# Kernel tuning notes

Hardware: AMD Instinct MI355X
Metric: run time of the kernel (lower is better)

## Reference

```python
import jax, jax.numpy as jnp
import numpy as np

D_MODEL = 1024
HEADS = 16
D_K = D_MODEL // HEADS


def setup_inputs() -> dict:
    key = jax.random.key(0)
    ks = jax.random.split(key, 12)
    B, S = 2, 2048
    scale = 1.0 / np.sqrt(D_MODEL)
    inp = {
        "q": jax.random.normal(ks[0], (B, S, D_MODEL), dtype=jnp.float32),
        "k": jax.random.normal(ks[1], (B, S, D_MODEL), dtype=jnp.float32),
        "v": jax.random.normal(ks[2], (B, S, D_MODEL), dtype=jnp.float32),
        "src_mask": jax.random.randint(ks[3], (B, 1, S), 0, 2, dtype=jnp.int32),
        # projection params (nn.Linear: y = x @ W.T + b); store W already transposed
        "Wq": jax.random.normal(ks[4], (D_MODEL, D_MODEL), dtype=jnp.float32) * scale,
        "bq": jnp.zeros((D_MODEL,), dtype=jnp.float32),
        "Wk": jax.random.normal(ks[5], (D_MODEL, D_MODEL), dtype=jnp.float32) * scale,
        "bk": jnp.zeros((D_MODEL,), dtype=jnp.float32),
        "Wv": jax.random.normal(ks[6], (D_MODEL, D_MODEL), dtype=jnp.float32) * scale,
        "bv": jnp.zeros((D_MODEL,), dtype=jnp.float32),
        "Wo": jax.random.normal(ks[7], (D_MODEL, D_MODEL), dtype=jnp.float32) * scale,
        "bo": jnp.zeros((D_MODEL,), dtype=jnp.float32),
    }
    return inp


def reference(q, k, v, src_mask, Wq, bq, Wk, bk, Wv, bv, Wo, bo):
    B, S, _ = q.shape
    # QKV projections, reshape to (b, heads, seq, d_k)
    def proj(x, W, b):
        y = x @ W + b  # (b, s, d_model)
        return y.reshape(B, S, HEADS, D_K).transpose(0, 2, 1, 3)

    qh = proj(q, Wq, bq)
    kh = proj(k, Wk, bk)
    vh = proj(v, Wv, bv)

    # scaled dot-product attention with padding mask
    scores = jnp.einsum("bhqd,bhkd->bhqk", qh, kh) / jnp.sqrt(jnp.float32(D_K))
    mask = src_mask[:, None, :, :]  # (b,1,1,s), broadcast over heads & query
    scores = jnp.where(mask == 0, jnp.float32(-1e9), scores)
    probs = jax.nn.softmax(scores, axis=-1)
    # dropout is identity in eval mode (reference baseline)
    ctx = jnp.einsum("bhqk,bhkd->bhqd", probs, vh)
    ctx = ctx.transpose(0, 2, 1, 3).reshape(B, S, D_MODEL)
    return ctx @ Wo + bo
```

## Files before the change

### kernel.cpp

```cpp
#include <hip/hip_runtime.h>
#include <hip/hip_bf16.h>

#define DM 1024
#define SL 2048
#define NH 16
#define DK 64

typedef __bf16 bf16;
typedef __bf16 bf16x8 __attribute__((ext_vector_type(8)));
typedef __bf16 bf16x4 __attribute__((ext_vector_type(4)));
typedef float f32x4 __attribute__((ext_vector_type(4)));
typedef float f32x16 __attribute__((ext_vector_type(16)));
typedef unsigned u32x4 __attribute__((ext_vector_type(4)));

__device__ __forceinline__ void gll16(const void* g, void* l) {
  __builtin_amdgcn_global_load_lds(
      (const __attribute__((address_space(1))) unsigned int*)g,
      (__attribute__((address_space(3))) unsigned int*)l, 16, 0, 0);
}

__device__ __forceinline__ unsigned pk2(float a, float b) {
  unsigned short lo = __builtin_bit_cast(unsigned short, (bf16)a);
  unsigned short hi = __builtin_bit_cast(unsigned short, (bf16)b);
  return (unsigned)lo | ((unsigned)hi << 16);
}

__global__ __launch_bounds__(256) void prep_kernel(
    const float* __restrict__ q, const float* __restrict__ k, const float* __restrict__ v,
    const float* __restrict__ Wq, const float* __restrict__ Wk,
    const float* __restrict__ Wv, const float* __restrict__ Wo,
    bf16* __restrict__ xq, bf16* __restrict__ xk, bf16* __restrict__ xv,
    bf16* __restrict__ TQ, bf16* __restrict__ TK, bf16* __restrict__ TV,
    bf16* __restrict__ TO) {
  __shared__ float t[64][65];
  const int bid = blockIdx.x, tid = threadIdx.x;
  if (bid < 6144) {
    const float* src; bf16* dst;
    if (bid < 2048)      { src = q; dst = xq; }
    else if (bid < 4096) { src = k; dst = xk; }
    else                 { src = v; dst = xv; }
    int i = (bid & 2047) * 2048 + tid * 8;
    f32x4 a = *(const f32x4*)(src + i);
    f32x4 b = *(const f32x4*)(src + i + 4);
    bf16x8 o;
    o[0]=(bf16)a[0]; o[1]=(bf16)a[1]; o[2]=(bf16)a[2]; o[3]=(bf16)a[3];
    o[4]=(bf16)b[0]; o[5]=(bf16)b[1]; o[6]=(bf16)b[2]; o[7]=(bf16)b[3];
    *(bf16x8*)(dst + i) = o;
  } else {
    const int wb = bid - 6144;
    const float* W; bf16* T;
    switch (wb >> 8) {
      case 0:  W = Wq; T = TQ; break;
      case 1:  W = Wk; T = TK; break;
      case 2:  W = Wv; T = TV; break;
      default: W = Wo; T = TO; break;
    }
    const int tile = wb & 255;
    const int tx = tile & 15, ty = tile >> 4;
    const int cr = tid >> 4, cc = tid & 15;
    #pragma unroll
    for (int rr = 0; rr < 4; ++rr) {
      int row = rr*16 + cr;
      f32x4 val = *(const f32x4*)(W + (ty*64 + row)*DM + tx*64 + cc*4);
      t[row][cc*4+0] = val[0]; t[row][cc*4+1] = val[1];
      t[row][cc*4+2] = val[2]; t[row][cc*4+3] = val[3];
    }
    __syncthreads();
    #pragma unroll
    for (int rr = 0; rr < 4; ++rr) {
      int nrow = rr*16 + cr;
      bf16x4 o;
      o[0] = (bf16)t[cc*4+0][nrow]; o[1] = (bf16)t[cc*4+1][nrow];
      o[2] = (bf16)t[cc*4+2][nrow]; o[3] = (bf16)t[cc*4+3][nrow];
      *(bf16x4*)(T + (tx*64 + nrow)*DM + ty*64 + cc*4) = o;
    }
  }
}

template<int MODE>
__device__ __forceinline__ void gemm_core(
    const bf16* __restrict__ A, const bf16* __restrict__ Bt, const float* __restrict__ bias,
    bf16* __restrict__ outH, float* __restrict__ outF) {
  const int bid = blockIdx.x;
  const int swz = (bid & 7) * 64 + (bid >> 3);
  const int mt = swz >> 3, nt = swz & 7;
  const int m0 = mt*64, n0 = nt*128;
  __shared__ __attribute__((aligned(16))) bf16 As[3][64*64];
  __shared__ __attribute__((aligned(16))) bf16 Bs[3][128*64];
  const int tid = threadIdx.x, lane = tid & 63, w = tid >> 6;
  const int wm = w >> 1, wn = w & 1;
  f32x4 acc[2][4];
  #pragma unroll
  for (int x = 0; x < 2; ++x)
    #pragma unroll
    for (int y = 0; y < 4; ++y)
      #pragma unroll
      for (int e = 0; e < 4; ++e) acc[x][y][e] = 0.f;

  #define GSTAGE(buf, kt_)                                                 \
    {                                                                      \
      const int k0s = (kt_)*64;                                            \
      _Pragma("unroll")                                                    \
      for (int i = 0; i < 2; ++i) {                                        \
        int idx = (i*4 + w)*64 + lane;                                     \
        int r = idx >> 3;                                                  \
        int s = (idx & 7) ^ (r & 7);                                       \
        gll16(A + (m0 + r)*DM + k0s + s*8, &As[buf][(i*4 + w)*512]);       \
      }                                                                    \
      _Pragma("unroll")                                                    \
      for (int i = 0; i < 4; ++i) {                                        \
        int idx = (i*4 + w)*64 + lane;                                     \
        int r = idx >> 3;                                                  \
        int s = (idx & 7) ^ (r & 7);                                       \
        gll16(Bt + (n0 + r)*DM + k0s + s*8, &Bs[buf][(i*4 + w)*512]);      \
      }                                                                    \
    }

  #define GCOMPUTE(cb)                                                             \
    {                                                                              \
      bf16x8 bfr[4][2];                                                            \
      _Pragma("unroll")                                                            \
      for (int ni = 0; ni < 4; ++ni) {                                             \
        int row = wn*64 + ni*16 + (lane & 15);                                     \
        _Pragma("unroll")                                                          \
        for (int c = 0; c < 2; ++c) {                                              \
          int slot = (lane >> 4) + c*4;                                            \
          bfr[ni][c] = *(const bf16x8*)&Bs[cb][row*64 + ((slot ^ (row & 7)) << 3)];\
        }                                                                          \
      }                                                                            \
      __builtin_amdgcn_s_setprio(1);                                               \
      _Pragma("unroll")                                                            \
      for (int mi = 0; mi < 2; ++mi) {                                             \
        int row = wm*32 + mi*16 + (lane & 15);                                     \
        bf16x8 a0 = *(const bf16x8*)&As[cb][row*64 + ((((lane >> 4)    ) ^ (row & 7)) << 3)]; \
        bf16x8 a1 = *(const bf16x8*)&As[cb][row*64 + ((((lane >> 4) + 4) ^ (row & 7)) << 3)]; \
        _Pragma("unroll")                                                          \
        for (int ni = 0; ni < 4; ++ni) {                                           \
          acc[mi][ni] = __builtin_amdgcn_mfma_f32_16x16x32_bf16(a0, bfr[ni][0], acc[mi][ni], 0, 0, 0); \
          acc[mi][ni] = __builtin_amdgcn_mfma_f32_16x16x32_bf16(a1, bfr[ni][1], acc[mi][ni], 0, 0, 0); \
        }                                                                          \
      }                                                                            \
      __builtin_amdgcn_s_setprio(0);                                               \
    }

  GSTAGE(0, 0);
  __syncthreads();
  int cur = 0;
  for (int kt = 0; kt < 15; ++kt) {
    int nxt = cur + 1; if (nxt == 3) nxt = 0;
    GSTAGE(nxt, kt + 1);
    asm volatile("s_waitcnt vmcnt(6)" ::: "memory");
    __builtin_amdgcn_s_barrier();
    GCOMPUTE(cur);
    cur = nxt;
  }
  asm volatile("s_waitcnt vmcnt(0)" ::: "memory");
  __builtin_amdgcn_s_barrier();
  GCOMPUTE(cur);
  #undef GSTAGE
  #undef GCOMPUTE

  #pragma unroll
  for (int ni = 0; ni < 4; ++ni) {
    int n = n0 + wn*64 + ni*16 + (lane & 15);
    float bv = bias[n];
    #pragma unroll
    for (int mi = 0; mi < 2; ++mi) {
      int mb = m0 + wm*32 + mi*16 + ((lane >> 4) << 2);
      if (MODE == 2) {
        int bb = mb >> 11, ss = mb & 2047, hh = n >> 6, dd = n & 63;
        bf16x4 o;
        #pragma unroll
        for (int j = 0; j < 4; ++j) o[j] = (bf16)(acc[mi][ni][j] + bv);
        *(bf16x4*)&outH[(((bb << 4) + hh)*DK + dd)*SL + ss] = o;
      } else {
        #pragma unroll
        for (int j = 0; j < 4; ++j) {
          int m = mb + j;
          float val = acc[mi][ni][j] + bv;
          if (MODE == 1) {
            int bb = m >> 11, ss = m & 2047, hh = n >> 6, dd = n & 63;
            outH[(((bb << 4) + hh)*SL + ss)*DK + dd] = (bf16)val;
          } else {
            outF[m*DM + n] = val;
          }
        }
      }
    }
  }
}

__global__ __launch_bounds__(256, 2) void proj_gemm_kernel(
    const bf16* XQ, const bf16* XK, const bf16* XV,
    const bf16* WTQp, const bf16* WTKp, const bf16* WTVp,
    const float* bq, const float* bk, const float* bv,
    bf16* QHp, bf16* KHp, bf16* VTp) {
  if (blockIdx.y == 0)      gemm_core<1>(XQ, WTQp, bq, QHp, nullptr);
  else if (blockIdx.y == 1) gemm_core<1>(XK, WTKp, bk, KHp, nullptr);
  else                      gemm_core<2>(XV, WTVp, bv, VTp, nullptr);
}

__global__ __launch_bounds__(256, 2) void out_gemm_kernel(
    const bf16* CTXp, const bf16* WTOp, const float* bo, float* out) {
  gemm_core<0>(CTXp, WTOp, bo, nullptr, out);
}

__global__ __launch_bounds__(256, 2) void attn_kernel(
    const bf16* __restrict__ QHp, const bf16* __restrict__ KHp,
    const bf16* __restrict__ VTp, const int* __restrict__ msk,
    bf16* __restrict__ CTXp) {
  const int d = blockIdx.x;
  const int xcd = d & 7, rr = d >> 3;
  const int bh = xcd*4 + (rr >> 4);
  const int qt = rr & 15;
  const int b = bh >> 4, h = bh & 15;
  const int q0 = qt * 128;
  const bf16* Qp  = QHp + bh * SL * DK;
  const bf16* Kp  = KHp + bh * SL * DK;
  const bf16* Vtp = VTp + bh * SL * DK;
  const int* mp = msk + b * SL;
  __shared__ __attribute__((aligned(16))) bf16 Ks[3][64*64];
  __shared__ __attribute__((aligned(16))) bf16 Vts[3][64*64];
  __shared__ __attribute__((aligned(16))) float mAdd[SL];
  const int tid = threadIdx.x, lane = tid & 63, w = tid >> 6;
  const int hi = lane >> 5, l5 = lane & 31;
  const float SCL2E = 0.18033688f;

  {
    int i0 = tid * 8;
    int4 a = *(const int4*)(mp + i0);
    int4 c = *(const int4*)(mp + i0 + 4);
    f32x4 oa, oc;
    oa[0] = a.x ? 0.f : -1.4426950e9f; oa[1] = a.y ? 0.f : -1.4426950e9f;
    oa[2] = a.z ? 0.f : -1.4426950e9f; oa[3] = a.w ? 0.f : -1.4426950e9f;
    oc[0] = c.x ? 0.f : -1.4426950e9f; oc[1] = c.y ? 0.f : -1.4426950e9f;
    oc[2] = c.z ? 0.f : -1.4426950e9f; oc[3] = c.w ? 0.f : -1.4426950e9f;
    *(f32x4*)&mAdd[i0] = oa;
    *(f32x4*)&mAdd[i0 + 4] = oc;
  }

  bf16x8 qf[4];
  {
    const bf16* qr = Qp + (q0 + w*32 + l5)*DK + hi*8;
    #pragma unroll
    for (int c = 0; c < 4; ++c) qf[c] = *(const bf16x8*)(qr + c*16);
  }
  f32x16 o0, o1;
  #pragma unroll
  for (int e = 0; e < 16; ++e) { o0[e] = 0.f; o1[e] = 0.f; }
  float m_run = -1e30f, l_run = 0.f;

  #define STAGE(buf, kt_)                                                  \
    {                                                                      \
      const int k0s = (kt_)*64;                                            \
      _Pragma("unroll")                                                    \
      for (int i = 0; i < 2; ++i) {                                        \
        int idx = (i*4 + w)*64 + lane;                                     \
        int r = idx >> 3;                                                  \
        int s = (idx & 7) ^ (r & 7);                                       \
        gll16(Kp + (k0s + r)*DK + s*8, &Ks[buf][(i*4 + w)*512]);           \
      }                                                                    \
      _Pragma("unroll")                                                    \
      for (int i = 0; i < 2; ++i) {                                        \
        int idx = (i*4 + w)*64 + lane;                                     \
        int r = idx >> 3;                                                  \
        int s = (idx & 7) ^ (r & 7);                                       \
        gll16(Vtp + r*SL + k0s + s*8, &Vts[buf][(i*4 + w)*512]);           \
      }                                                                    \
    }

  #define ATILE(cb, k0)                                                          \
    {                                                                            \
      f32x16 s0, s1;                                                             \
      _Pragma("unroll")                                                          \
      for (int e = 0; e < 16; ++e) { s0[e] = 0.f; s1[e] = 0.f; }                 \
      __builtin_amdgcn_s_setprio(1);                                             \
      _Pragma("unroll")                                                          \
      for (int c = 0; c < 4; ++c) {                                              \
        int sl = 2*c + hi;                                                       \
        int r0 = l5, r1 = 32 + l5;                                               \
        bf16x8 kf0 = *(const bf16x8*)&Ks[cb][r0*64 + ((sl ^ (r0 & 7)) << 3)];    \
        bf16x8 kf1 = *(const bf16x8*)&Ks[cb][r1*64 + ((sl ^ (r1 & 7)) << 3)];    \
        s0 = __builtin_amdgcn_mfma_f32_32x32x16_bf16(kf0, qf[c], s0, 0, 0, 0);   \
        s1 = __builtin_amdgcn_mfma_f32_32x32x16_bf16(kf1, qf[c], s1, 0, 0, 0);   \
      }                                                                          \
      __builtin_amdgcn_s_setprio(0);                                             \
      float pv_[32];                                                             \
      float mtv0 = -1e30f, mtv1 = -1e30f, mtv2 = -1e30f, mtv3 = -1e30f;          \
      _Pragma("unroll")                                                          \
      for (int half = 0; half < 2; ++half) {                                     \
        _Pragma("unroll")                                                        \
        for (int qd = 0; qd < 4; ++qd) {                                         \
          f32x4 ma = *(const f32x4*)&mAdd[(k0) + half*32 + qd*8 + hi*4];         \
          _Pragma("unroll")                                                      \
          for (int j = 0; j < 4; ++j) {                                          \
            float val = (half ? s1[qd*4+j] : s0[qd*4+j]) * SCL2E + ma[j];        \
            pv_[half*16 + qd*4 + j] = val;                                       \
            if (j == 0) mtv0 = fmaxf(mtv0, val);                                 \
            else if (j == 1) mtv1 = fmaxf(mtv1, val);                            \
            else if (j == 2) mtv2 = fmaxf(mtv2, val);                            \
            else mtv3 = fmaxf(mtv3, val);                                        \
          }                                                                      \
        }                                                                        \
      }                                                                          \
      float mt = fmaxf(fmaxf(mtv0, mtv1), fmaxf(mtv2, mtv3));                    \
      mt = fmaxf(mt, __shfl_xor(mt, 32));                                        \
      if (!__all(mt - m_run <= 11.5f)) {                                         \
        float mnew = fmaxf(m_run, mt);                                           \
        float sf = exp2f(m_run - mnew);                                          \
        _Pragma("unroll")                                                        \
        for (int reg = 0; reg < 16; ++reg) {                                     \
          int crow = (reg & 3) + ((reg >> 2) << 3) + (hi << 2);                  \
          float s_ = __shfl(sf, crow);                                           \
          o0[reg] *= s_; o1[reg] *= s_;                                          \
        }                                                                        \
        l_run *= sf;                                                             \
        m_run = mnew;                                                            \
      }                                                                          \
      float ls0 = 0.f, ls1 = 0.f, ls2 = 0.f, ls3 = 0.f;                          \
      _Pragma("unroll")                                                          \
      for (int t = 0; t < 32; ++t) {                                             \
        float p = exp2f(pv_[t] - m_run);                                         \
        pv_[t] = p;                                                              \
        if ((t & 3) == 0) ls0 += p;                                              \
        else if ((t & 3) == 1) ls1 += p;                                         \
        else if ((t & 3) == 2) ls2 += p;                                         \
        else ls3 += p;                                                           \
      }                                                                          \
      float lsum = (ls0 + ls1) + (ls2 + ls3);                                    \
      lsum += __shfl_xor(lsum, 32);                                              \
      l_run += lsum;                                                             \
      _Pragma("unroll")                                                          \
      for (int c = 0; c < 4; ++c) {                                              \
        const int half_c = c >> 1;                                               \
        const int iA = half_c*16 + (((2*c)    ) & 3)*4;                          \
        const int iB = half_c*16 + (((2*c) + 1) & 3)*4;                          \
        unsigned wA0 = pk2(pv_[iA],   pv_[iA+1]);                                \
        unsigned wA1 = pk2(pv_[iA+2], pv_[iA+3]);                                \
        unsigned wB0 = pk2(pv_[iB],   pv_[iB+1]);                                \
        unsigned wB1 = pk2(pv_[iB+2], pv_[iB+3]);                                \
        unsigned ow0 = hi ? wB0 : wA0, ow1 = hi ? wB1 : wA1;                     \
        unsigned xw0 = hi ? wA0 : wB0, xw1 = hi ? wA1 : wB1;                     \
        unsigned yw0 = __shfl_xor(xw0, 32);                                      \
        unsigned yw1 = __shfl_xor(xw1, 32);                                      \
        u32x4 uu;                                                                \
        uu[0] = hi ? yw0 : ow0;                                                  \
        uu[1] = hi ? yw1 : ow1;                                                  \
        uu[2] = hi ? ow0 : yw0;                                                  \
        uu[3] = hi ? ow1 : yw1;                                                  \
        bf16x8 pa = __builtin_bit_cast(bf16x8, uu);                              \
        int sl = 2*c + hi;                                                       \
        int r0 = l5, r1 = 32 + l5;                                               \
        bf16x8 vf0 = *(const bf16x8*)&Vts[cb][r0*64 + ((sl ^ (r0 & 7)) << 3)];   \
        bf16x8 vf1 = *(const bf16x8*)&Vts[cb][r1*64 + ((sl ^ (r1 & 7)) << 3)];   \
        __builtin_amdgcn_s_setprio(1);                                           \
        o0 = __builtin_amdgcn_mfma_f32_32x32x16_bf16(pa, vf0, o0, 0, 0, 0);      \
        o1 = __builtin_amdgcn_mfma_f32_32x32x16_bf16(pa, vf1, o1, 0, 0, 0);      \
        __builtin_amdgcn_s_setprio(0);                                           \
      }                                                                          \
    }

  STAGE(0, 0);
  __syncthreads();
  int cur = 0;
  for (int kt = 0; kt < 31; ++kt) {
    int nxt = cur + 1; if (nxt == 3) nxt = 0;
    STAGE(nxt, kt + 1);
    asm volatile("s_waitcnt vmcnt(4)" ::: "memory");
    __builtin_amdgcn_s_barrier();
    ATILE(cur, kt*64);
    cur = nxt;
  }
  asm volatile("s_waitcnt vmcnt(0)" ::: "memory");
  __builtin_amdgcn_s_barrier();
  ATILE(cur, 31*64);
  #undef STAGE
  #undef ATILE

  float inv = 1.f / l_run;
  const int sbase = (b * SL) * DM + h * DK;
  #pragma unroll
  for (int reg = 0; reg < 16; ++reg) {
    int crow = (reg & 3) + ((reg >> 2) << 3) + (hi << 2);
    float iv = __shfl(inv, crow);
    int srow = q0 + w*32 + crow;
    CTXp[sbase + srow*DM + l5]      = (bf16)(o0[reg] * iv);
    CTXp[sbase + srow*DM + 32 + l5] = (bf16)(o1[reg] * iv);
  }
}

extern "C" void kernel_launch(void* const* d_in, const int* in_sizes, int n_in,
                              void* d_out, int out_size, void* d_ws, size_t ws_size,
                              hipStream_t stream) {
  const float* q  = (const float*)d_in[0];
  const float* k  = (const float*)d_in[1];
  const float* v  = (const float*)d_in[2];
  const int*  msk = (const int*)d_in[3];
  const float* Wq = (const float*)d_in[4];
  const float* bq = (const float*)d_in[5];
  const float* Wk = (const float*)d_in[6];
  const float* bk = (const float*)d_in[7];
  const float* Wv = (const float*)d_in[8];
  const float* bv = (const float*)d_in[9];
  const float* Wo = (const float*)d_in[10];
  const float* bo = (const float*)d_in[11];
  char* ws = (char*)d_ws;
  bf16* XQ  = (bf16*)(ws + 0);
  bf16* XK  = (bf16*)(ws + 8388608);
  bf16* XV  = (bf16*)(ws + 16777216);
  bf16* WTQ = (bf16*)(ws + 25165824);
  bf16* WTK = (bf16*)(ws + 27262976);
  bf16* WTV = (bf16*)(ws + 29360128);
  bf16* WTO = (bf16*)(ws + 31457280);
  bf16* QHb = (bf16*)(ws + 33554432);
  bf16* KHb = (bf16*)(ws + 41943040);
  bf16* VTb = (bf16*)(ws + 50331648);
  bf16* CTX = (bf16*)(ws + 58720256);
  float* out = (float*)d_out;

  prep_kernel<<<dim3(7168), 256, 0, stream>>>(q, k, v, Wq, Wk, Wv, Wo,
                                              XQ, XK, XV, WTQ, WTK, WTV, WTO);
  proj_gemm_kernel<<<dim3(512, 3), 256, 0, stream>>>(XQ, XK, XV, WTQ, WTK, WTV,
                                                     bq, bk, bv, QHb, KHb, VTb);
  attn_kernel<<<dim3(512), 256, 0, stream>>>(QHb, KHb, VTb, msk, CTX);
  out_gemm_kernel<<<dim3(512), 256, 0, stream>>>(CTX, WTO, bo, out);
}
```

Measured before the change: 268.2 us.

## Compact unmasked keys/values and skip masked key tiles in attention

Adds a mask prefix-scan kernel that gathers the indices of unmasked key positions. The prep kernel uses them to pack K and V rows densely, so attention only loops over ceil(nv/64) key tiles and masks by index, not by a per-key table. With random masks about half the keys are masked, so this is meant to remove roughly half the attention work. The GEMM and attention pipelines are also restructured to prefetch two stages ahead. It stores scratch indices in the output buffer, which out_gemm later overwrites, and it still projects all padded rows.

Result: faster. 230.4 us (-14.1%).

```diff
diff --git a/kernel.cpp b/kernel.cpp
--- a/kernel.cpp
+++ b/kernel.cpp
@@ -25,27 +25,69 @@
   return (unsigned)lo | ((unsigned)hi << 16);
 }
 
+__global__ __launch_bounds__(256) void mask_scan_kernel(
+    const int* __restrict__ msk, int* __restrict__ gidx, int* __restrict__ nvp) {
+  const int b = blockIdx.x, tid = threadIdx.x;
+  const int* mp = msk + b * SL;
+  __shared__ int ssum[256];
+  int loc[8]; int cnt = 0;
+  #pragma unroll
+  for (int j = 0; j < 8; ++j) { loc[j] = (mp[tid*8 + j] != 0); cnt += loc[j]; }
+  ssum[tid] = cnt;
+  __syncthreads();
+  for (int off = 1; off < 256; off <<= 1) {
+    int v = ssum[tid];
+    int vv = (tid >= off) ? ssum[tid - off] : 0;
+    __syncthreads();
+    ssum[tid] = v + vv;
+    __syncthreads();
+  }
+  int base = ssum[tid] - cnt;
+  #pragma unroll
+  for (int j = 0; j < 8; ++j) {
+    if (loc[j]) gidx[b*SL + base++] = tid*8 + j;
+  }
+  if (tid == 255) nvp[b] = ssum[255];
+}
+
 __global__ __launch_bounds__(256) void prep_kernel(
     const float* __restrict__ q, const float* __restrict__ k, const float* __restrict__ v,
     const float* __restrict__ Wq, const float* __restrict__ Wk,
     const float* __restrict__ Wv, const float* __restrict__ Wo,
     bf16* __restrict__ xq, bf16* __restrict__ xk, bf16* __restrict__ xv,
     bf16* __restrict__ TQ, bf16* __restrict__ TK, bf16* __restrict__ TV,
-    bf16* __restrict__ TO) {
+    bf16* __restrict__ TO,
+    const int* __restrict__ gidx, const int* __restrict__ nvp) {
   __shared__ float t[64][65];
   const int bid = blockIdx.x, tid = threadIdx.x;
-  if (bid < 6144) {
-    const float* src; bf16* dst;
-    if (bid < 2048)      { src = q; dst = xq; }
-    else if (bid < 4096) { src = k; dst = xk; }
-    else                 { src = v; dst = xv; }
-    int i = (bid & 2047) * 2048 + tid * 8;
-    f32x4 a = *(const f32x4*)(src + i);
-    f32x4 b = *(const f32x4*)(src + i + 4);
+  if (bid < 2048) {
+    int i = bid * 2048 + tid * 8;
+    f32x4 a = *(const f32x4*)(q + i);
+    f32x4 b2 = *(const f32x4*)(q + i + 4);
     bf16x8 o;
     o[0]=(bf16)a[0]; o[1]=(bf16)a[1]; o[2]=(bf16)a[2]; o[3]=(bf16)a[3];
-    o[4]=(bf16)b[0]; o[5]=(bf16)b[1]; o[6]=(bf16)b[2]; o[7]=(bf16)b[3];
-    *(bf16x8*)(dst + i) = o;
+    o[4]=(bf16)b2[0]; o[5]=(bf16)b2[1]; o[6]=(bf16)b2[2]; o[7]=(bf16)b2[3];
+    *(bf16x8*)(xq + i) = o;
+  } else if (bid < 6144) {
+    const int isV = (bid >= 4096);
+    const float* src = isV ? v : k;
+    bf16* dst = isV ? xv : xk;
+    const int orow = ((bid - (isV ? 4096 : 2048)) << 1) + (tid >> 7);
+    const int bb = orow >> 11, j = orow & 2047;
+    const int col = (tid & 127) * 8;
+    bf16x8 o;
+    if (j < nvp[bb]) {
+      int sr = gidx[bb*SL + j];
+      const float* rp = src + (bb*SL + sr)*DM + col;
+      f32x4 a = *(const f32x4*)rp;
+      f32x4 b2 = *(const f32x4*)(rp + 4);
+      o[0]=(bf16)a[0]; o[1]=(bf16)a[1]; o[2]=(bf16)a[2]; o[3]=(bf16)a[3];
+      o[4]=(bf16)b2[0]; o[5]=(bf16)b2[1]; o[6]=(bf16)b2[2]; o[7]=(bf16)b2[3];
+    } else {
+      #pragma unroll
+      for (int e = 0; e < 8; ++e) o[e] = (bf16)0.f;
+    }
+    *(bf16x8*)(dst + orow*DM + col) = o;
   } else {
     const int wb = bid - 6144;
     const float* W; bf16* T;
@@ -80,13 +122,12 @@
 template<int MODE>
 __device__ __forceinline__ void gemm_core(
     const bf16* __restrict__ A, const bf16* __restrict__ Bt, const float* __restrict__ bias,
-    bf16* __restrict__ outH, float* __restrict__ outF) {
+    bf16* __restrict__ outH, float* __restrict__ outF,
+    bf16* As, bf16* Bs) {
   const int bid = blockIdx.x;
   const int swz = (bid & 7) * 64 + (bid >> 3);
   const int mt = swz >> 3, nt = swz & 7;
   const int m0 = mt*64, n0 = nt*128;
-  __shared__ __attribute__((aligned(16))) bf16 As[3][64*64];
-  __shared__ __attribute__((aligned(16))) bf16 Bs[3][128*64];
   const int tid = threadIdx.x, lane = tid & 63, w = tid >> 6;
   const int wm = w >> 1, wn = w & 1;
   f32x4 acc[2][4];
@@ -97,66 +138,65 @@
       #pragma unroll
       for (int e = 0; e < 4; ++e) acc[x][y][e] = 0.f;
 
-  #define GSTAGE(buf, kt_)                                                 \
-    {                                                                      \
-      const int k0s = (kt_)*64;                                            \
-      _Pragma("unroll")                                                    \
-      for (int i = 0; i < 2; ++i) {                                        \
-        int idx = (i*4 + w)*64 + lane;                                     \
-        int r = idx >> 3;                                                  \
-        int s = (idx & 7) ^ (r & 7);                                       \
-        gll16(A + (m0 + r)*DM + k0s + s*8, &As[buf][(i*4 + w)*512]);       \
-      }                                                                    \
-      _Pragma("unroll")                                                    \
-      for (int i = 0; i < 4; ++i) {                                        \
-        int idx = (i*4 + w)*64 + lane;                                     \
-        int r = idx >> 3;                                                  \
-        int s = (idx & 7) ^ (r & 7);                                       \
-        gll16(Bt + (n0 + r)*DM + k0s + s*8, &Bs[buf][(i*4 + w)*512]);      \
-      }                                                                    \
-    }
-
-  #define GCOMPUTE(cb)                                                             \
-    {                                                                              \
-      bf16x8 bfr[4][2];                                                            \
-      _Pragma("unroll")                                                            \
-      for (int ni = 0; ni < 4; ++ni) {                                             \
-        int row = wn*64 + ni*16 + (lane & 15);                                     \
-        _Pragma("unroll")                                                          \
-        for (int c = 0; c < 2; ++c) {                                              \
-          int slot = (lane >> 4) + c*4;                                            \
-          bfr[ni][c] = *(const bf16x8*)&Bs[cb][row*64 + ((slot ^ (row & 7)) << 3)];\
-        }                                                                          \
-      }                                                                            \
-      __builtin_amdgcn_s_setprio(1);                                               \
-      _Pragma("unroll")                                                            \
-      for (int mi = 0; mi < 2; ++mi) {                                             \
-        int row = wm*32 + mi*16 + (lane & 15);                                     \
-        bf16x8 a0 = *(const bf16x8*)&As[cb][row*64 + ((((lane >> 4)    ) ^ (row & 7)) << 3)]; \
-        bf16x8 a1 = *(const bf16x8*)&As[cb][row*64 + ((((lane >> 4) + 4) ^ (row & 7)) << 3)]; \
-        _Pragma("unroll")                                                          \
-        for (int ni = 0; ni < 4; ++ni) {                                           \
+  #define GSTAGE(buf, kt_)                                                  \
+    {                                                                       \
+      const int k0s = (kt_)*64;                                             \
+      _Pragma("unroll")                                                     \
+      for (int i = 0; i < 2; ++i) {                                         \
+        int idx = (i*4 + w)*64 + lane;                                      \
+        int r = idx >> 3;                                                   \
+        int s = (idx & 7) ^ (r & 7);                                        \
+        gll16(A + (m0 + r)*DM + k0s + s*8, &As[(buf)*4096 + (i*4 + w)*512]);\
+      }                                                                     \
+      _Pragma("unroll")                                                     \
+      for (int i = 0; i < 4; ++i) {                                         \
+        int idx = (i*4 + w)*64 + lane;                                      \
+        int r = idx >> 3;                                                   \
+        int s = (idx & 7) ^ (r & 7);                                        \
+        gll16(Bt + (n0 + r)*DM + k0s + s*8, &Bs[(buf)*8192 + (i*4 + w)*512]);\
+      }                                                                     \
+    }
+
+  #define GCOMPUTE(cb)                                                              \
+    {                                                                               \
+      bf16x8 bfr[4][2];                                                             \
+      _Pragma("unroll")                                                             \
+      for (int ni = 0; ni < 4; ++ni) {                                              \
+        int row = wn*64 + ni*16 + (lane & 15);                                      \
+        _Pragma("unroll")                                                           \
+        for (int c = 0; c < 2; ++c) {                                               \
+          int slot = (lane >> 4) + c*4;                                             \
+          bfr[ni][c] = *(const bf16x8*)&Bs[(cb)*8192 + row*64 + ((slot ^ (row & 7)) << 3)]; \
+        }                                                                           \
+      }                                                                             \
+      __builtin_amdgcn_s_setprio(1);                                                \
+      _Pragma("unroll")                                                             \
+      for (int mi = 0; mi < 2; ++mi) {                                              \
+        int row = wm*32 + mi*16 + (lane & 15);                                      \
+        bf16x8 a0 = *(const bf16x8*)&As[(cb)*4096 + row*64 + ((((lane >> 4)    ) ^ (row & 7)) << 3)]; \
+        bf16x8 a1 = *(const bf16x8*)&As[(cb)*4096 + row*64 + ((((lane >> 4) + 4) ^ (row & 7)) << 3)]; \
+        _Pragma("unroll")                                                           \
+        for (int ni = 0; ni < 4; ++ni) {                                            \
           acc[mi][ni] = __builtin_amdgcn_mfma_f32_16x16x32_bf16(a0, bfr[ni][0], acc[mi][ni], 0, 0, 0); \
           acc[mi][ni] = __builtin_amdgcn_mfma_f32_16x16x32_bf16(a1, bfr[ni][1], acc[mi][ni], 0, 0, 0); \
-        }                                                                          \
-      }                                                                            \
-      __builtin_amdgcn_s_setprio(0);                                               \
+        }                                                                           \
+      }                                                                             \
+      __builtin_amdgcn_s_setprio(0);                                                \
     }
 
   GSTAGE(0, 0);
+  GSTAGE(1, 1);
   __syncthreads();
   int cur = 0;
-  for (int kt = 0; kt < 15; ++kt) {
-    int nxt = cur + 1; if (nxt == 3) nxt = 0;
-    GSTAGE(nxt, kt + 1);
-    asm volatile("s_waitcnt vmcnt(6)" ::: "memory");
-    __builtin_amdgcn_s_barrier();
+  for (int kt = 0; kt < 16; ++kt) {
+    asm volatile("s_waitcnt vmcnt(6)\n\ts_barrier" ::: "memory");
+    int nb = cur + 2; if (nb >= 3) nb -= 3;
+    int kts = kt + 2; if (kts > 15) kts = 15;
+    GSTAGE(nb, kts);
     GCOMPUTE(cur);
-    cur = nxt;
+    ++cur; if (cur == 3) cur = 0;
   }
   asm volatile("s_waitcnt vmcnt(0)" ::: "memory");
-  __builtin_amdgcn_s_barrier();
-  GCOMPUTE(cur);
   #undef GSTAGE
   #undef GCOMPUTE
 
@@ -195,19 +235,23 @@
     const bf16* WTQp, const bf16* WTKp, const bf16* WTVp,
     const float* bq, const float* bk, const float* bv,
     bf16* QHp, bf16* KHp, bf16* VTp) {
-  if (blockIdx.y == 0)      gemm_core<1>(XQ, WTQp, bq, QHp, nullptr);
-  else if (blockIdx.y == 1) gemm_core<1>(XK, WTKp, bk, KHp, nullptr);
-  else                      gemm_core<2>(XV, WTVp, bv, VTp, nullptr);
+  __shared__ __attribute__((aligned(16))) bf16 As[3*64*64];
+  __shared__ __attribute__((aligned(16))) bf16 Bs[3*128*64];
+  if (blockIdx.y == 0)      gemm_core<1>(XQ, WTQp, bq, QHp, nullptr, As, Bs);
+  else if (blockIdx.y == 1) gemm_core<1>(XK, WTKp, bk, KHp, nullptr, As, Bs);
+  else                      gemm_core<2>(XV, WTVp, bv, VTp, nullptr, As, Bs);
 }
 
 __global__ __launch_bounds__(256, 2) void out_gemm_kernel(
     const bf16* CTXp, const bf16* WTOp, const float* bo, float* out) {
-  gemm_core<0>(CTXp, WTOp, bo, nullptr, out);
+  __shared__ __attribute__((aligned(16))) bf16 As[3*64*64];
+  __shared__ __attribute__((aligned(16))) bf16 Bs[3*128*64];
+  gemm_core<0>(CTXp, WTOp, bo, nullptr, out, As, Bs);
 }
 
 __global__ __launch_bounds__(256, 2) void attn_kernel(
     const bf16* __restrict__ QHp, const bf16* __restrict__ KHp,
-    const bf16* __restrict__ VTp, const int* __restrict__ msk,
+    const bf16* __restrict__ VTp, const int* __restrict__ nvp,
     bf16* __restrict__ CTXp) {
   const int d = blockIdx.x;
   const int xcd = d & 7, rr = d >> 3;
@@ -218,26 +262,14 @@
   const bf16* Qp  = QHp + bh * SL * DK;
   const bf16* Kp  = KHp + bh * SL * DK;
   const bf16* Vtp = VTp + bh * SL * DK;
-  const int* mp = msk + b * SL;
   __shared__ __attribute__((aligned(16))) bf16 Ks[3][64*64];
   __shared__ __attribute__((aligned(16))) bf16 Vts[3][64*64];
-  __shared__ __attribute__((aligned(16))) float mAdd[SL];
   const int tid = threadIdx.x, lane = tid & 63, w = tid >> 6;
   const int hi = lane >> 5, l5 = lane & 31;
   const float SCL2E = 0.18033688f;
 
-  {
-    int i0 = tid * 8;
-    int4 a = *(const int4*)(mp + i0);
-    int4 c = *(const int4*)(mp + i0 + 4);
-    f32x4 oa, oc;
-    oa[0] = a.x ? 0.f : -1.4426950e9f; oa[1] = a.y ? 0.f : -1.4426950e9f;
-    oa[2] = a.z ? 0.f : -1.4426950e9f; oa[3] = a.w ? 0.f : -1.4426950e9f;
-    oc[0] = c.x ? 0.f : -1.4426950e9f; oc[1] = c.y ? 0.f : -1.4426950e9f;
-    oc[2] = c.z ? 0.f : -1.4426950e9f; oc[3] = c.w ? 0.f : -1.4426950e9f;
-    *(f32x4*)&mAdd[i0] = oa;
-    *(f32x4*)&mAdd[i0 + 4] = oc;
-  }
+  const int nv = nvp[b];
+  int ntile = (nv + 63) >> 6; if (ntile < 1) ntile = 1;
 
   bf16x8 qf[4];
   {
@@ -291,10 +323,11 @@
       for (int half = 0; half < 2; ++half) {                                     \
         _Pragma("unroll")                                                        \
         for (int qd = 0; qd < 4; ++qd) {                                         \
-          f32x4 ma = *(const f32x4*)&mAdd[(k0) + half*32 + qd*8 + hi*4];         \
           _Pragma("unroll")                                                      \
           for (int j = 0; j < 4; ++j) {                                          \
-            float val = (half ? s1[qd*4+j] : s0[qd*4+j]) * SCL2E + ma[j];        \
+            float val = (half ? s1[qd*4+j] : s0[qd*4+j]) * SCL2E;                \
+            int key = (k0) + half*32 + qd*8 + hi*4 + j;                          \
+            val = (key < nv) ? val : -1.0e9f;                                    \
             pv_[half*16 + qd*4 + j] = val;                                       \
             if (j == 0) mtv0 = fmaxf(mtv0, val);                                 \
             else if (j == 1) mtv1 = fmaxf(mtv1, val);                            \
@@ -361,19 +394,18 @@
     }
 
   STAGE(0, 0);
+  { int t1 = (ntile > 1) ? 1 : 0; STAGE(1, t1); }
   __syncthreads();
   int cur = 0;
-  for (int kt = 0; kt < 31; ++kt) {
-    int nxt = cur + 1; if (nxt == 3) nxt = 0;
-    STAGE(nxt, kt + 1);
-    asm volatile("s_waitcnt vmcnt(4)" ::: "memory");
-    __builtin_amdgcn_s_barrier();
+  for (int kt = 0; kt < ntile; ++kt) {
+    asm volatile("s_waitcnt vmcnt(4)\n\ts_barrier" ::: "memory");
+    int nb = cur + 2; if (nb >= 3) nb -= 3;
+    int kts = kt + 2; if (kts > ntile - 1) kts = ntile - 1;
+    STAGE(nb, kts);
     ATILE(cur, kt*64);
-    cur = nxt;
+    ++cur; if (cur == 3) cur = 0;
   }
   asm volatile("s_waitcnt vmcnt(0)" ::: "memory");
-  __builtin_amdgcn_s_barrier();
-  ATILE(cur, 31*64);
   #undef STAGE
   #undef ATILE
 
@@ -417,11 +449,15 @@
   bf16* VTb = (bf16*)(ws + 50331648);
   bf16* CTX = (bf16*)(ws + 58720256);
   float* out = (float*)d_out;
-
+  int* gidx = (int*)d_out;
+  int* nvp  = (int*)((char*)d_out + 16384);
+
+  mask_scan_kernel<<<dim3(2), 256, 0, stream>>>(msk, gidx, nvp);
   prep_kernel<<<dim3(7168), 256, 0, stream>>>(q, k, v, Wq, Wk, Wv, Wo,
-                                              XQ, XK, XV, WTQ, WTK, WTV, WTO);
+                                              XQ, XK, XV, WTQ, WTK, WTV, WTO,
+                                              gidx, nvp);
   proj_gemm_kernel<<<dim3(512, 3), 256, 0, stream>>>(XQ, XK, XV, WTQ, WTK, WTV,
                                                      bq, bk, bv, QHb, KHb, VTb);
-  attn_kernel<<<dim3(512), 256, 0, stream>>>(QHb, KHb, VTb, msk, CTX);
+  attn_kernel<<<dim3(512), 256, 0, stream>>>(QHb, KHb, VTb, nvp, CTX);
   out_gemm_kernel<<<dim3(512), 256, 0, stream>>>(CTX, WTO, bo, out);
 }
```
